# Kernel optimization log

Measured on AMD Instinct MI355X. Metric: run time of the kernel, lower is better.

The kernel has to match this reference:

```python
import jax, jax.numpy as jnp
import numpy as np

S, IN, OUT = 32, 2048, 2048


def setup_inputs() -> dict:
    key = jax.random.key(0)
    k1, k2, k3 = jax.random.split(key, 3)
    lim = 1.0 / np.sqrt(IN)
    return {
        "x": jax.random.normal(k1, (S, IN), dtype=jnp.float32),
        "weight_mu": jax.random.uniform(k2, (OUT, IN), dtype=jnp.float32, minval=-lim, maxval=lim),
        "weight_sigma": jnp.full((OUT, IN), 0.1, dtype=jnp.float32),
        "bias_mu": jax.random.uniform(k3, (OUT,), dtype=jnp.float32, minval=-lim, maxval=lim),
        "bias_sigma": jnp.full((OUT,), 0.1, dtype=jnp.float32),
        "samples": S,
    }


def reference(x, weight_mu, weight_sigma, bias_mu, bias_sigma, samples):
    # Reparameterized sampling: w = mu + sigma * eps, eps ~ N(0,1), one weight per sample.
    key = jax.random.key(42)
    wkey, bkey = jax.random.split(key)
    eps_w = jax.random.normal(wkey, (samples,) + weight_mu.shape, dtype=weight_mu.dtype)  # (S, OUT, IN)
    weights = weight_mu + weight_sigma * eps_w  # (S, OUT, IN)
    # Per-sample matvec: out[s] = weights[s] @ x[s]
    out = jnp.einsum("soi,si->so", weights, x)  # (S, OUT)
    eps_b = jax.random.normal(bkey, (samples,) + bias_mu.shape, dtype=bias_mu.dtype)  # (S, OUT)
    out = out + (bias_mu + bias_sigma * eps_b)
    return out
```

## Files before the change

kernel.cpp:

```cpp
#include <hip/hip_runtime.h>
#include <stdint.h>

#define NS 32
#define NIN 2048
#define NOUT 2048


#define ADD4                                 \
    "v_add_u32 %[t0], %[t0], %[a0]\n\t"      \
    "v_add_u32 %[t1], %[t1], %[a1]\n\t"      \
    "v_add_u32 %[t2], %[t2], %[a2]\n\t"      \
    "v_add_u32 %[t3], %[t3], %[a3]\n\t"

#define ADDK4                                \
    "v_add_u32 %[t0], %[k0], %[a0]\n\t"      \
    "v_add_u32 %[t1], %[k0], %[a1]\n\t"      \
    "v_add_u32 %[t2], %[k0], %[a2]\n\t"      \
    "v_add_u32 %[t3], %[k0], %[a3]\n\t"

#define ROT4(sh)                                          \
    "v_alignbit_b32 %[a0], %[a0], %[a0], " sh "\n\t"      \
    "v_alignbit_b32 %[a1], %[a1], %[a1], " sh "\n\t"      \
    "v_alignbit_b32 %[a2], %[a2], %[a2], " sh "\n\t"      \
    "v_alignbit_b32 %[a3], %[a3], %[a3], " sh "\n\t"

#define XOR4                                 \
    "v_xor_b32 %[a0], %[a0], %[t0]\n\t"      \
    "v_xor_b32 %[a1], %[a1], %[t1]\n\t"      \
    "v_xor_b32 %[a2], %[a2], %[t2]\n\t"      \
    "v_xor_b32 %[a3], %[a3], %[t3]\n\t"

#define TF4R(sh) ADD4 ROT4(sh) XOR4

#define TF4INJ(ka, kb)                           \
    "v_add_u32 %[t0], %[" ka "], %[t0]\n\t"      \
    "v_add_u32 %[t1], %[" ka "], %[t1]\n\t"      \
    "v_add_u32 %[t2], %[" ka "], %[t2]\n\t"      \
    "v_add_u32 %[t3], %[" ka "], %[t3]\n\t"      \
    "v_add_u32 %[a0], %[" kb "], %[a0]\n\t"      \
    "v_add_u32 %[a1], %[" kb "], %[a1]\n\t"      \
    "v_add_u32 %[a2], %[" kb "], %[a2]\n\t"      \
    "v_add_u32 %[a3], %[" kb "], %[a3]\n\t"

__device__ __forceinline__ void tf_fold4(uint32_t k0, uint32_t k1, uint32_t k2,
                                         uint32_t& a0, uint32_t& a1,
                                         uint32_t& a2, uint32_t& a3) {
    uint32_t t0, t1, t2, t3;
    const uint32_t c1 = k2 + 1u, c2 = k0 + 2u, c3 = k1 + 3u, c4 = k2 + 4u, c5 = k0 + 5u;
    asm volatile(
        ADDK4 ROT4("19") XOR4
        TF4R("17") TF4R("6") TF4R("26")
        TF4INJ("k1", "c1")
        TF4R("15") TF4R("3") TF4R("16") TF4R("8")
        TF4INJ("k2", "c2")
        TF4R("19") TF4R("17") TF4R("6") TF4R("26")
        TF4INJ("k0", "c3")
        TF4R("15") TF4R("3") TF4R("16") TF4R("8")
        TF4INJ("k1", "c4")
        TF4R("19") TF4R("17") TF4R("6") TF4R("26")
        TF4INJ("k2", "c5")
        XOR4
        : [a0] "+v"(a0), [a1] "+v"(a1), [a2] "+v"(a2), [a3] "+v"(a3),
          [t0] "=&v"(t0), [t1] "=&v"(t1), [t2] "=&v"(t2), [t3] "=&v"(t3)
        : [k0] "s"(k0), [k1] "s"(k1), [k2] "s"(k2),
          [c1] "s"(c1), [c2] "s"(c2), [c3] "s"(c3), [c4] "s"(c4), [c5] "s"(c5));
}

__device__ __forceinline__ void uw_from_bits(uint32_t bits, float& u, float& w) {
    const float LO = __uint_as_float(0xBF7FFFFFu);
    float f = __uint_as_float((bits >> 9) | 0x3f800000u) - 1.0f;
    u = fmaf(f, 2.0f, LO);
    w = -__logf(fmaf(-u, u, 1.0f));
}

__device__ __forceinline__ float erfinv_p_fast(float w) {
    float t = w - 2.5f;
    float p = 2.81022636e-08f;
    p = fmaf(p, t, 3.43273939e-07f);
    p = fmaf(p, t, -3.5233877e-06f);
    p = fmaf(p, t, -4.39150654e-06f);
    p = fmaf(p, t, 0.00021858087f);
    p = fmaf(p, t, -0.00125372503f);
    p = fmaf(p, t, -0.00417768164f);
    p = fmaf(p, t, 0.246640727f);
    p = fmaf(p, t, 1.50140941f);
    return p;
}

__device__ __forceinline__ float erfinv_p_slow(float w) {
    float t = __fsqrt_rn(w) - 3.0f;
    float p = -0.000200214257f;
    p = fmaf(p, t, 0.000100950558f);
    p = fmaf(p, t, 0.00134934322f);
    p = fmaf(p, t, -0.00367342844f);
    p = fmaf(p, t, 0.00573950773f);
    p = fmaf(p, t, -0.0076224613f);
    p = fmaf(p, t, 0.00943887047f);
    p = fmaf(p, t, 1.00167406f);
    p = fmaf(p, t, 2.83297682f);
    return p;
}

__device__ __forceinline__ float normal_from_bits(uint32_t bits) {
    float u, w;
    uw_from_bits(bits, u, w);
    float p = (w < 5.0f) ? erfinv_p_fast(w) : erfinv_p_slow(w);
    return 1.41421356237f * p * u;
}

__global__ __launch_bounds__(256, 2) void bayes_linear_kernel(
    const float* __restrict__ x, const float* __restrict__ wmu,
    const float* __restrict__ wsg, const float* __restrict__ bmu,
    const float* __restrict__ bsg, float* __restrict__ out,
    uint32_t kw0, uint32_t kw1, uint32_t kb0, uint32_t kb1) {
    const int o = blockIdx.x;
    const int tid = threadIdx.x;
    const int s = tid & 31;
    const int g = tid >> 5;

    const uint32_t kw2 = kw0 ^ kw1 ^ 0x1BD11BDAu;
    const uint32_t kb2 = kb0 ^ kb1 ^ 0x1BD11BDAu;

    const uint32_t baseo = (uint32_t)o * NIN;
    const uint32_t ibase = (uint32_t)g * (NIN / 8);
    const uint32_t pb0 = (uint32_t)s * (uint32_t)(NOUT * NIN) + baseo + ibase + kw1;

    const float4* __restrict__ wmu4 = (const float4*)(wmu + baseo + ibase);
    const float4* __restrict__ wsg4 = (const float4*)(wsg + baseo + ibase);
    const float4* __restrict__ xp4  = (const float4*)(x + (uint32_t)s * NIN + ibase);

    float acc0 = 0.0f, acc1 = 0.0f;
    for (int it = 0; it < NIN / 8 / 4; ++it) {
        const float4 m4 = wmu4[it];
        const float4 g4 = wsg4[it];
        const float4 xv = xp4[it];

        const uint32_t p = pb0 + (uint32_t)(it * 4);
        uint32_t b0 = p + 0u, b1 = p + 1u, b2 = p + 2u, b3 = p + 3u;
        tf_fold4(kw0, kw1, kw2, b0, b1, b2, b3);

        float u0, u1, u2, u3, w0, w1, w2, w3;
        uw_from_bits(b0, u0, w0);
        uw_from_bits(b1, u1, w1);
        uw_from_bits(b2, u2, w2);
        uw_from_bits(b3, u3, w3);
        float p0 = erfinv_p_fast(w0);
        float p1 = erfinv_p_fast(w1);
        float p2 = erfinv_p_fast(w2);
        float p3 = erfinv_p_fast(w3);
        if (__any(fmaxf(fmaxf(w0, w1), fmaxf(w2, w3)) >= 5.0f)) {
            if (w0 >= 5.0f) p0 = erfinv_p_slow(w0);
            if (w1 >= 5.0f) p1 = erfinv_p_slow(w1);
            if (w2 >= 5.0f) p2 = erfinv_p_slow(w2);
            if (w3 >= 5.0f) p3 = erfinv_p_slow(w3);
        }
        const float e0 = 1.41421356237f * p0 * u0;
        const float e1 = 1.41421356237f * p1 * u1;
        const float e2 = 1.41421356237f * p2 * u2;
        const float e3 = 1.41421356237f * p3 * u3;

        acc0 = fmaf(fmaf(g4.x, e0, m4.x), xv.x, acc0);
        acc1 = fmaf(fmaf(g4.y, e1, m4.y), xv.y, acc1);
        acc0 = fmaf(fmaf(g4.z, e2, m4.z), xv.z, acc0);
        acc1 = fmaf(fmaf(g4.w, e3, m4.w), xv.w, acc1);
    }

    __shared__ float red[8][NS];
    red[g][s] = acc0 + acc1;
    __syncthreads();

    if (tid < NS) {
        const int ss = tid;
        float sum = 0.0f;
#pragma unroll
        for (int gg = 0; gg < 8; ++gg) sum += red[gg][ss];
        const uint32_t pb = (uint32_t)(ss * NOUT + o) + kb1;
        uint32_t b0 = pb, b1 = pb, b2 = pb, b3 = pb;
        tf_fold4(kb0, kb1, kb2, b0, b1, b2, b3);
        const float eb = normal_from_bits(b0);
        out[ss * NOUT + o] = sum + fmaf(bsg[o], eb, bmu[o]);
    }
}

#define TF_ROUND_H(x0, x1, r)                     \
    do {                                          \
        x0 += x1;                                 \
        x1 = (x1 << (r)) | (x1 >> (32 - (r)));    \
        x1 ^= x0;                                 \
    } while (0)

static void tf2x32_host(uint32_t k0, uint32_t k1, uint32_t x0, uint32_t x1,
                        uint32_t* y0, uint32_t* y1) {
    uint32_t k2 = k0 ^ k1 ^ 0x1BD11BDAu;
    x0 += k0; x1 += k1;
    TF_ROUND_H(x0, x1, 13); TF_ROUND_H(x0, x1, 15); TF_ROUND_H(x0, x1, 26); TF_ROUND_H(x0, x1, 6);
    x0 += k1; x1 += k2 + 1u;
    TF_ROUND_H(x0, x1, 17); TF_ROUND_H(x0, x1, 29); TF_ROUND_H(x0, x1, 16); TF_ROUND_H(x0, x1, 24);
    x0 += k2; x1 += k0 + 2u;
    TF_ROUND_H(x0, x1, 13); TF_ROUND_H(x0, x1, 15); TF_ROUND_H(x0, x1, 26); TF_ROUND_H(x0, x1, 6);
    x0 += k0; x1 += k1 + 3u;
    TF_ROUND_H(x0, x1, 17); TF_ROUND_H(x0, x1, 29); TF_ROUND_H(x0, x1, 16); TF_ROUND_H(x0, x1, 24);
    x0 += k1; x1 += k2 + 4u;
    TF_ROUND_H(x0, x1, 13); TF_ROUND_H(x0, x1, 15); TF_ROUND_H(x0, x1, 26); TF_ROUND_H(x0, x1, 6);
    x0 += k2; x1 += k0 + 5u;
    *y0 = x0; *y1 = x1;
}

extern "C" void kernel_launch(void* const* d_in, const int* in_sizes, int n_in,
                              void* d_out, int out_size, void* d_ws, size_t ws_size,
                              hipStream_t stream) {
    const float* x   = (const float*)d_in[0];
    const float* wmu = (const float*)d_in[1];
    const float* wsg = (const float*)d_in[2];
    const float* bmu = (const float*)d_in[3];
    const float* bsg = (const float*)d_in[4];
    float* out = (float*)d_out;

    uint32_t kw0, kw1, kb0, kb1;
    tf2x32_host(0u, 42u, 0u, 0u, &kw0, &kw1);
    tf2x32_host(0u, 42u, 0u, 1u, &kb0, &kb1);

    bayes_linear_kernel<<<NOUT, 256, 0, stream>>>(x, wmu, wsg, bmu, bsg, out,
                                                  kw0, kw1, kb0, kb1);
}
```

Baseline: 338.1 us.

## Remap work to one wavefront per sample-output pair with shuffle reduction

The grid becomes 8x larger. Each 64-lane wavefront now computes one (sample, output) dot product with coalesced float4 loads over the input dimension, and reduces with wavefront shuffles instead of shared memory and a block barrier. The erfinv polynomials are refolded to take log2 directly with the sqrt(2) factor absorbed into the coefficients, which removes a multiply and the log scaling per element. Launch bounds are raised to 6 blocks per CU and the asm is made non-volatile so the compiler can schedule it. The trade-off is that wmu/wsg rows are now reloaded by 8 blocks instead of 1, and register pressure rises from the full unroll.

```diff
diff --git a/kernel.cpp b/kernel.cpp
--- a/kernel.cpp
+++ b/kernel.cpp
@@ -47,8 +47,7 @@
                                          uint32_t& a2, uint32_t& a3) {
     uint32_t t0, t1, t2, t3;
     const uint32_t c1 = k2 + 1u, c2 = k0 + 2u, c3 = k1 + 3u, c4 = k2 + 4u, c5 = k0 + 5u;
-    asm volatile(
-        ADDK4 ROT4("19") XOR4
+    asm(ADDK4 ROT4("19") XOR4
         TF4R("17") TF4R("6") TF4R("26")
         TF4INJ("k1", "c1")
         TF4R("15") TF4R("3") TF4R("16") TF4R("8")
@@ -66,119 +65,142 @@
           [c1] "s"(c1), [c2] "s"(c2), [c3] "s"(c3), [c4] "s"(c4), [c5] "s"(c5));
 }
 
-__device__ __forceinline__ void uw_from_bits(uint32_t bits, float& u, float& w) {
+__device__ __forceinline__ void ul2_from_bits(uint32_t bits, float& u, float& l2) {
     const float LO = __uint_as_float(0xBF7FFFFFu);
     float f = __uint_as_float((bits >> 9) | 0x3f800000u) - 1.0f;
     u = fmaf(f, 2.0f, LO);
-    w = -__logf(fmaf(-u, u, 1.0f));
-}
-
-__device__ __forceinline__ float erfinv_p_fast(float w) {
-    float t = w - 2.5f;
-    float p = 2.81022636e-08f;
-    p = fmaf(p, t, 3.43273939e-07f);
-    p = fmaf(p, t, -3.5233877e-06f);
-    p = fmaf(p, t, -4.39150654e-06f);
-    p = fmaf(p, t, 0.00021858087f);
-    p = fmaf(p, t, -0.00125372503f);
-    p = fmaf(p, t, -0.00417768164f);
-    p = fmaf(p, t, 0.246640727f);
-    p = fmaf(p, t, 1.50140941f);
+    l2 = __log2f(fmaf(-u, u, 1.0f));
+}
+
+__device__ __forceinline__ float erfinv2_fast(float l2) {
+    float t = fmaf(l2, -0.69314718f, -2.5f);
+    float p = 3.9739403e-08f;
+    p = fmaf(p, t, 4.8546628e-07f);
+    p = fmaf(p, t, -4.9828418e-06f);
+    p = fmaf(p, t, -6.2105079e-06f);
+    p = fmaf(p, t, 3.0912069e-04f);
+    p = fmaf(p, t, -1.7730336e-03f);
+    p = fmaf(p, t, -5.9081371e-03f);
+    p = fmaf(p, t, 0.34878364f);
+    p = fmaf(p, t, 2.1233153f);
     return p;
 }
 
-__device__ __forceinline__ float erfinv_p_slow(float w) {
+__device__ __forceinline__ float erfinv2_slow(float l2) {
+    float w = l2 * -0.69314718f;
     float t = __fsqrt_rn(w) - 3.0f;
-    float p = -0.000200214257f;
-    p = fmaf(p, t, 0.000100950558f);
-    p = fmaf(p, t, 0.00134934322f);
-    p = fmaf(p, t, -0.00367342844f);
-    p = fmaf(p, t, 0.00573950773f);
-    p = fmaf(p, t, -0.0076224613f);
-    p = fmaf(p, t, 0.00943887047f);
-    p = fmaf(p, t, 1.00167406f);
-    p = fmaf(p, t, 2.83297682f);
+    float p = -2.8314685e-04f;
+    p = fmaf(p, t, 1.4276577e-04f);
+    p = fmaf(p, t, 1.9082652e-03f);
+    p = fmaf(p, t, -5.1950077e-03f);
+    p = fmaf(p, t, 8.1169428e-03f);
+    p = fmaf(p, t, -1.0779843e-02f);
+    p = fmaf(p, t, 1.3348618e-02f);
+    p = fmaf(p, t, 1.4165813f);
+    p = fmaf(p, t, 4.0064342f);
     return p;
 }
 
+__device__ __forceinline__ uint32_t rotl32c(uint32_t v, uint32_t r) {
+    return __builtin_amdgcn_alignbit(v, v, 32u - r);
+}
+#define TF_R1(x0, x1, r) do { x0 += x1; x1 = rotl32c(x1, r) ^ x0; } while (0)
+__device__ __forceinline__ uint32_t tf_fold1(uint32_t k0, uint32_t k1, uint32_t k2,
+                                             uint32_t x1in) {
+    uint32_t x0 = k0 + x1in;
+    uint32_t x1 = rotl32c(x1in, 13) ^ x0;
+    TF_R1(x0, x1, 15); TF_R1(x0, x1, 26); TF_R1(x0, x1, 6);
+    x0 += k1; x1 += k2 + 1u;
+    TF_R1(x0, x1, 17); TF_R1(x0, x1, 29); TF_R1(x0, x1, 16); TF_R1(x0, x1, 24);
+    x0 += k2; x1 += k0 + 2u;
+    TF_R1(x0, x1, 13); TF_R1(x0, x1, 15); TF_R1(x0, x1, 26); TF_R1(x0, x1, 6);
+    x0 += k0; x1 += k1 + 3u;
+    TF_R1(x0, x1, 17); TF_R1(x0, x1, 29); TF_R1(x0, x1, 16); TF_R1(x0, x1, 24);
+    x0 += k1; x1 += k2 + 4u;
+    TF_R1(x0, x1, 13); TF_R1(x0, x1, 15); TF_R1(x0, x1, 26); TF_R1(x0, x1, 6);
+    x0 += k2; x1 += k0 + 5u;
+    return x0 ^ x1;
+}
+
 __device__ __forceinline__ float normal_from_bits(uint32_t bits) {
-    float u, w;
-    uw_from_bits(bits, u, w);
-    float p = (w < 5.0f) ? erfinv_p_fast(w) : erfinv_p_slow(w);
-    return 1.41421356237f * p * u;
-}
-
-__global__ __launch_bounds__(256, 2) void bayes_linear_kernel(
+    float u, l2;
+    ul2_from_bits(bits, u, l2);
+    float p = (l2 > -7.2134752f) ? erfinv2_fast(l2) : erfinv2_slow(l2);
+    return p * u;
+}
+
+__global__ __launch_bounds__(256, 6) void bayes_linear_kernel(
     const float* __restrict__ x, const float* __restrict__ wmu,
     const float* __restrict__ wsg, const float* __restrict__ bmu,
     const float* __restrict__ bsg, float* __restrict__ out,
     uint32_t kw0, uint32_t kw1, uint32_t kb0, uint32_t kb1) {
-    const int o = blockIdx.x;
-    const int tid = threadIdx.x;
-    const int s = tid & 31;
-    const int g = tid >> 5;
+    const uint32_t bid = blockIdx.x;
+    const uint32_t o = bid >> 3;
+    const uint32_t sg = bid & 7u;
+    const uint32_t tid = threadIdx.x;
+    const uint32_t wv = tid >> 6;
+    const uint32_t lane = tid & 63u;
+    const uint32_t s = sg * 4u + wv;
 
     const uint32_t kw2 = kw0 ^ kw1 ^ 0x1BD11BDAu;
     const uint32_t kb2 = kb0 ^ kb1 ^ 0x1BD11BDAu;
 
-    const uint32_t baseo = (uint32_t)o * NIN;
-    const uint32_t ibase = (uint32_t)g * (NIN / 8);
-    const uint32_t pb0 = (uint32_t)s * (uint32_t)(NOUT * NIN) + baseo + ibase + kw1;
-
-    const float4* __restrict__ wmu4 = (const float4*)(wmu + baseo + ibase);
-    const float4* __restrict__ wsg4 = (const float4*)(wsg + baseo + ibase);
-    const float4* __restrict__ xp4  = (const float4*)(x + (uint32_t)s * NIN + ibase);
-
-    float acc0 = 0.0f, acc1 = 0.0f;
-    for (int it = 0; it < NIN / 8 / 4; ++it) {
-        const float4 m4 = wmu4[it];
-        const float4 g4 = wsg4[it];
-        const float4 xv = xp4[it];
-
-        const uint32_t p = pb0 + (uint32_t)(it * 4);
-        uint32_t b0 = p + 0u, b1 = p + 1u, b2 = p + 2u, b3 = p + 3u;
+    const uint32_t pbase = s * (uint32_t)(NOUT * NIN) + o * (uint32_t)NIN +
+                           kw1 + lane * 4u;
+
+    const float4* __restrict__ mp = (const float4*)(wmu + o * NIN) + lane;
+    const float4* __restrict__ gp = (const float4*)(wsg + o * NIN) + lane;
+    const float4* __restrict__ xp = (const float4*)(x + s * NIN) + lane;
+
+    float ax = 0.0f, ay = 0.0f, az = 0.0f, aw = 0.0f;
+#pragma unroll
+    for (int it = 0; it < 8; ++it) {
+        const float4 m4 = mp[it * 64];
+        const float4 g4 = gp[it * 64];
+        const float4 x4 = xp[it * 64];
+
+        const uint32_t p = pbase + (uint32_t)(it * 256);
+        uint32_t b0 = p, b1 = p + 1u, b2 = p + 2u, b3 = p + 3u;
         tf_fold4(kw0, kw1, kw2, b0, b1, b2, b3);
 
-        float u0, u1, u2, u3, w0, w1, w2, w3;
-        uw_from_bits(b0, u0, w0);
-        uw_from_bits(b1, u1, w1);
-        uw_from_bits(b2, u2, w2);
-        uw_from_bits(b3, u3, w3);
-        float p0 = erfinv_p_fast(w0);
-        float p1 = erfinv_p_fast(w1);
-        float p2 = erfinv_p_fast(w2);
-        float p3 = erfinv_p_fast(w3);
-        if (__any(fmaxf(fmaxf(w0, w1), fmaxf(w2, w3)) >= 5.0f)) {
-            if (w0 >= 5.0f) p0 = erfinv_p_slow(w0);
-            if (w1 >= 5.0f) p1 = erfinv_p_slow(w1);
-            if (w2 >= 5.0f) p2 = erfinv_p_slow(w2);
-            if (w3 >= 5.0f) p3 = erfinv_p_slow(w3);
+        float u0, u1, u2, u3, l0, l1, l2v, l3;
+        ul2_from_bits(b0, u0, l0);
+        ul2_from_bits(b1, u1, l1);
+        ul2_from_bits(b2, u2, l2v);
+        ul2_from_bits(b3, u3, l3);
+        float p0 = erfinv2_fast(l0);
+        float p1 = erfinv2_fast(l1);
+        float p2 = erfinv2_fast(l2v);
+        float p3 = erfinv2_fast(l3);
+        if (__any(fminf(fminf(l0, l1), fminf(l2v, l3)) <= -7.2134752f)) {
+            if (l0 <= -7.2134752f) p0 = erfinv2_slow(l0);
+            if (l1 <= -7.2134752f) p1 = erfinv2_slow(l1);
+            if (l2v <= -7.2134752f) p2 = erfinv2_slow(l2v);
+            if (l3 <= -7.2134752f) p3 = erfinv2_slow(l3);
         }
-        const float e0 = 1.41421356237f * p0 * u0;
-        const float e1 = 1.41421356237f * p1 * u1;
-        const float e2 = 1.41421356237f * p2 * u2;
-        const float e3 = 1.41421356237f * p3 * u3;
-
-        acc0 = fmaf(fmaf(g4.x, e0, m4.x), xv.x, acc0);
-        acc1 = fmaf(fmaf(g4.y, e1, m4.y), xv.y, acc1);
-        acc0 = fmaf(fmaf(g4.z, e2, m4.z), xv.z, acc0);
-        acc1 = fmaf(fmaf(g4.w, e3, m4.w), xv.w, acc1);
+        const float e0 = p0 * u0;
+        const float e1 = p1 * u1;
+        const float e2 = p2 * u2;
+        const float e3 = p3 * u3;
+
+        ax = fmaf(fmaf(g4.x, e0, m4.x), x4.x, ax);
+        ay = fmaf(fmaf(g4.y, e1, m4.y), x4.y, ay);
+        az = fmaf(fmaf(g4.z, e2, m4.z), x4.z, az);
+        aw = fmaf(fmaf(g4.w, e3, m4.w), x4.w, aw);
     }
 
-    __shared__ float red[8][NS];
-    red[g][s] = acc0 + acc1;
-    __syncthreads();
-
-    if (tid < NS) {
-        const int ss = tid;
-        float sum = 0.0f;
-#pragma unroll
-        for (int gg = 0; gg < 8; ++gg) sum += red[gg][ss];
-        const uint32_t pb = (uint32_t)(ss * NOUT + o) + kb1;
-        uint32_t b0 = pb, b1 = pb, b2 = pb, b3 = pb;
-        tf_fold4(kb0, kb1, kb2, b0, b1, b2, b3);
-        const float eb = normal_from_bits(b0);
-        out[ss * NOUT + o] = sum + fmaf(bsg[o], eb, bmu[o]);
+    float v = (ax + ay) + (az + aw);
+    v += __shfl_down(v, 32, 64);
+    v += __shfl_down(v, 16, 64);
+    v += __shfl_down(v, 8, 64);
+    v += __shfl_down(v, 4, 64);
+    v += __shfl_down(v, 2, 64);
+    v += __shfl_down(v, 1, 64);
+
+    if (lane == 0) {
+        const uint32_t pb = s * (uint32_t)NOUT + o + kb1;
+        const float eb = normal_from_bits(tf_fold1(kb0, kb1, kb2, pb));
+        out[s * NOUT + o] = v + fmaf(bsg[o], eb, bmu[o]);
     }
 }
 
@@ -220,6 +242,6 @@
     tf2x32_host(0u, 42u, 0u, 0u, &kw0, &kw1);
     tf2x32_host(0u, 42u, 0u, 1u, &kb0, &kb1);
 
-    bayes_linear_kernel<<<NOUT, 256, 0, stream>>>(x, wmu, wsg, bmu, bsg, out,
-                                                  kw0, kw1, kb0, kb1);
-}
+    bayes_linear_kernel<<<NOUT * 8, 256, 0, stream>>>(x, wmu, wsg, bmu, bsg, out,
+                                                      kw0, kw1, kb0, kb1);
+}
```

Result: slower. 484.4 us (+43.3%).
